# Kernel tuning notes

Hardware: AMD Instinct MI355X
Metric: run time of the kernel (lower is better)

## Reference

```python
import jax, jax.numpy as jnp
import numpy as np

SIREN_OMEGA_0 = 30.0
EPS = 1e-4


def setup_inputs() -> dict:
    key = jax.random.key(0)
    ks = jax.random.split(key, 10)
    B, N, M, IN, OUT = 2, 16384, 1024, 256, 256
    x = jax.random.normal(ks[0], (B, N, IN), dtype=jnp.float32)
    query_coords = jax.random.normal(ks[1], (B, N, 3), dtype=jnp.float32)
    atomic_coords = jax.random.normal(ks[2], (B, M, 3), dtype=jnp.float32)
    # SIREN init (not is_first): bound = sqrt(6/in)/omega_0
    bound = (6.0 / IN) ** 0.5 / SIREN_OMEGA_0
    W = jax.random.uniform(ks[3], (OUT, IN), jnp.float32, -bound, bound)
    b = jax.random.uniform(ks[4], (OUT,), jnp.float32, -bound, bound)
    # freq_net: Linear(3,16) -> Softplus -> Linear(16,1), default torch init
    b1l = 1.0 / np.sqrt(3.0)
    fw1 = jax.random.uniform(ks[5], (16, 3), jnp.float32, -b1l, b1l)
    fb1 = jax.random.uniform(ks[6], (16,), jnp.float32, -b1l, b1l)
    b2l = 1.0 / np.sqrt(16.0)
    fw2 = jax.random.uniform(ks[7], (1, 16), jnp.float32, -b2l, b2l)
    fb2 = jax.random.uniform(ks[8], (1,), jnp.float32, -b2l, b2l)
    return {"x": x, "query_coords": query_coords, "atomic_coords": atomic_coords,
            "W": W, "b": b, "fw1": fw1, "fb1": fb1, "fw2": fw2, "fb2": fb2}


def reference(x, query_coords, atomic_coords, W, b, fw1, fb1, fw2, fb2):
    omega_base = SIREN_OMEGA_0
    # pre_activation = x @ W^T + b : [B, N, OUT]
    pre = jnp.einsum('bni,oi->bno', x, W) + b
    # freq_net(query_coords): Linear -> softplus -> Linear, clamp [0,5], nan->0
    h = jax.nn.softplus(jnp.einsum('bnd,hd->bnh', query_coords, fw1) + fb1)
    local_scale = jnp.einsum('bnh,oh->bno', h, fw2) + fb2  # [B, N, 1]
    local_scale = jnp.nan_to_num(jnp.clip(local_scale, 0.0, 5.0), nan=0.0)
    # pairwise distance [B, N, M] via broadcasted diff, then min over atoms
    diff = query_coords[:, :, None, :] - atomic_coords[:, None, :, :]  # [B,N,M,3]
    dist = jnp.sqrt(jnp.maximum(jnp.sum(diff * diff, axis=-1), EPS))
    min_dist = jnp.min(dist, axis=-1, keepdims=True)  # [B, N, 1]
    omega = omega_base * (1.0 + local_scale * jnp.exp(-min_dist))
    return jnp.sin(omega * pre)
```

## Files before the change

### kernel.cpp

```cpp
#include <hip/hip_runtime.h>
#include <hip/hip_bf16.h>

#define NPTS    32768
#define K_DIM   256
#define O_DIM   256
#define M_ATOMS 1024

typedef __attribute__((ext_vector_type(8))) short short8;
typedef __attribute__((ext_vector_type(4))) float f32x4;

__device__ __forceinline__ void split1(float v, short* h, short* l) {
  unsigned short hu = __bfloat16_as_ushort(__float2bfloat16(v));
  *h = (short)hu;
  float r = v - __uint_as_float((unsigned)hu << 16);
  *l = (short)__bfloat16_as_ushort(__float2bfloat16(r));
}

__device__ __forceinline__ void cvt8(const f32x4 f0, const f32x4 f1,
                                     short8* h, short8* l) {
#pragma unroll
  for (int j = 0; j < 4; ++j) {
    short hh, ll;
    split1(f0[j], &hh, &ll);
    (*h)[j] = hh; (*l)[j] = ll;
    split1(f1[j], &hh, &ll);
    (*h)[j + 4] = hh; (*l)[j + 4] = ll;
  }
}

__global__ __launch_bounds__(256) void wprep_kernel(const float* __restrict__ W,
                                                    unsigned short* __restrict__ whF,
                                                    unsigned short* __restrict__ wlF) {
  int t = blockIdx.x * 256 + threadIdx.x;
  int lane = t & 63;
  int ct = (t >> 6) & 15;
  int kc = t >> 10;
  int col = ct * 16 + (lane & 15);
  int k0 = kc * 32 + (lane >> 4) * 8;
  const float* src = W + (size_t)col * K_DIM + k0;
  f32x4 f0 = *(const f32x4*)(src);
  f32x4 f1 = *(const f32x4*)(src + 4);
  short8 h, l;
  cvt8(f0, f1, &h, &l);
  *(short8*)(whF + (size_t)t * 8) = h;
  *(short8*)(wlF + (size_t)t * 8) = l;
}

__global__ __launch_bounds__(256, 2) void fused_kernel(
    const float* __restrict__ x, const float* __restrict__ qc,
    const float* __restrict__ atoms,
    const unsigned short* __restrict__ whF, const unsigned short* __restrict__ wlF,
    const float* __restrict__ bias,
    const float* __restrict__ fw1, const float* __restrict__ fb1,
    const float* __restrict__ fw2, const float* __restrict__ fb2,
    float* __restrict__ out) {
  __shared__ f32x4 at4[M_ATOMS];
  __shared__ float red[4][64];
  __shared__ float omg[64];

  const int tid = threadIdx.x;
  const int lane = tid & 63;
  const int w = tid >> 6;
  const int lrow = lane & 15;
  const int lk = lane >> 4;
  const int pbase = blockIdx.x * 64;

  const short8* BH = (const short8*)whF + (size_t)(w * 4) * 64 + lane;
  const short8* BL = (const short8*)wlF + (size_t)(w * 4) * 64 + lane;
  short8 bh[4], bl[4], nh[4], nl[4];
#pragma unroll
  for (int ct = 0; ct < 4; ++ct) {
    bh[ct] = BH[ct * 64];
    bl[ct] = BL[ct * 64];
  }
  const float* xr = x + (size_t)(pbase + lrow) * K_DIM + lk * 8;
  f32x4 r0[4], r1[4];
#pragma unroll
  for (int t = 0; t < 4; ++t) {
    r0[t] = *(const f32x4*)(xr + t * 16 * K_DIM);
    r1[t] = *(const f32x4*)(xr + t * 16 * K_DIM + 4);
  }

  const int batch = pbase >> 14;
  const float* A = atoms + (size_t)batch * M_ATOMS * 3;
#pragma unroll
  for (int j = 0; j < 4; ++j) {
    int i = tid + j * 256;
    const float* ap = A + (size_t)i * 3;
    float ax = ap[0], ay = ap[1], az = ap[2];
    at4[i] = (f32x4){ax, ay, az, ax * ax + ay * ay + az * az};
  }
  __syncthreads();

  const int pt = pbase + lane;
  const float qx = qc[(size_t)pt * 3 + 0];
  const float qy = qc[(size_t)pt * 3 + 1];
  const float qz = qc[(size_t)pt * 3 + 2];
  {
    float m0 = 3.0e38f, m1 = 3.0e38f, m2 = 3.0e38f, m3 = 3.0e38f;
    const int i0 = w * 256;
    for (int i = i0; i < i0 + 256; i += 4) {
      f32x4 v0 = at4[i + 0], v1 = at4[i + 1], v2 = at4[i + 2], v3 = at4[i + 3];
      float d;
      d = v0[0] * qx; d = __fmaf_rn(v0[1], qy, d); d = __fmaf_rn(v0[2], qz, d);
      m0 = fminf(m0, __fmaf_rn(d, -2.0f, v0[3]));
      d = v1[0] * qx; d = __fmaf_rn(v1[1], qy, d); d = __fmaf_rn(v1[2], qz, d);
      m1 = fminf(m1, __fmaf_rn(d, -2.0f, v1[3]));
      d = v2[0] * qx; d = __fmaf_rn(v2[1], qy, d); d = __fmaf_rn(v2[2], qz, d);
      m2 = fminf(m2, __fmaf_rn(d, -2.0f, v2[3]));
      d = v3[0] * qx; d = __fmaf_rn(v3[1], qy, d); d = __fmaf_rn(v3[2], qz, d);
      m3 = fminf(m3, __fmaf_rn(d, -2.0f, v3[3]));
    }
    red[w][lane] = fminf(fminf(m0, m1), fminf(m2, m3));
  }
  __syncthreads();
  if (w == 0) {
    float md = fminf(fminf(red[0][lane], red[1][lane]),
                     fminf(red[2][lane], red[3][lane]));
    md += qx * qx + qy * qy + qz * qz;
    float mind = sqrtf(fmaxf(md, 1.0e-4f));
    float facc = fb2[0];
#pragma unroll
    for (int j = 0; j < 16; ++j) {
      float z = fw1[j * 3 + 0] * qx + fw1[j * 3 + 1] * qy + fw1[j * 3 + 2] * qz + fb1[j];
      facc += fw2[j] * (fmaxf(z, 0.0f) + __logf(1.0f + __expf(-fabsf(z))));
    }
    float ls = fminf(fmaxf(facc, 0.0f), 5.0f);
    omg[lane] = 30.0f * (1.0f + ls * __expf(-mind));
  }
  __syncthreads();

  short8 ahi[4], alo[4];
#pragma unroll
  for (int t = 0; t < 4; ++t) cvt8(r0[t], r1[t], &ahi[t], &alo[t]);

  f32x4 acc[4][4];
#pragma unroll
  for (int t = 0; t < 4; ++t)
#pragma unroll
    for (int ct = 0; ct < 4; ++ct) acc[t][ct] = (f32x4){0.f, 0.f, 0.f, 0.f};

#pragma unroll 2
  for (int kc = 0; kc < 8; ++kc) {
    if (kc < 7) {
#pragma unroll
      for (int ct = 0; ct < 4; ++ct) {
        nh[ct] = BH[(kc + 1) * 1024 + ct * 64];
        nl[ct] = BL[(kc + 1) * 1024 + ct * 64];
      }
#pragma unroll
      for (int t = 0; t < 4; ++t) {
        r0[t] = *(const f32x4*)(xr + t * 16 * K_DIM + (kc + 1) * 32);
        r1[t] = *(const f32x4*)(xr + t * 16 * K_DIM + (kc + 1) * 32 + 4);
      }
    }
#pragma unroll
    for (int ct = 0; ct < 4; ++ct)
#pragma unroll
      for (int t = 0; t < 4; ++t)
        acc[t][ct] = __builtin_amdgcn_mfma_f32_16x16x32_bf16(ahi[t], bh[ct], acc[t][ct], 0, 0, 0);
#pragma unroll
    for (int ct = 0; ct < 4; ++ct)
#pragma unroll
      for (int t = 0; t < 4; ++t)
        acc[t][ct] = __builtin_amdgcn_mfma_f32_16x16x32_bf16(alo[t], bh[ct], acc[t][ct], 0, 0, 0);
#pragma unroll
    for (int ct = 0; ct < 4; ++ct)
#pragma unroll
      for (int t = 0; t < 4; ++t)
        acc[t][ct] = __builtin_amdgcn_mfma_f32_16x16x32_bf16(ahi[t], bl[ct], acc[t][ct], 0, 0, 0);
    if (kc < 7) {
#pragma unroll
      for (int t = 0; t < 4; ++t) cvt8(r0[t], r1[t], &ahi[t], &alo[t]);
#pragma unroll
      for (int ct = 0; ct < 4; ++ct) { bh[ct] = nh[ct]; bl[ct] = nl[ct]; }
    }
  }

#pragma unroll
  for (int ct = 0; ct < 4; ++ct) {
    float bv = bias[w * 64 + ct * 16 + lrow];
#pragma unroll
    for (int t = 0; t < 4; ++t) {
#pragma unroll
      for (int j = 0; j < 4; ++j) {
        float om = omg[t * 16 + lk * 4 + j];
        float pre = acc[t][ct][j] + bv;
        out[(size_t)(pbase + t * 16 + lk * 4 + j) * O_DIM + w * 64 + ct * 16 + lrow] =
            __sinf(om * pre);
      }
    }
  }
}

extern "C" void kernel_launch(void* const* d_in, const int* in_sizes, int n_in,
                              void* d_out, int out_size, void* d_ws, size_t ws_size,
                              hipStream_t stream) {
  (void)in_sizes; (void)n_in; (void)out_size; (void)ws_size;
  const float* x     = (const float*)d_in[0];
  const float* qc    = (const float*)d_in[1];
  const float* atoms = (const float*)d_in[2];
  const float* W     = (const float*)d_in[3];
  const float* b     = (const float*)d_in[4];
  const float* fw1   = (const float*)d_in[5];
  const float* fb1   = (const float*)d_in[6];
  const float* fw2   = (const float*)d_in[7];
  const float* fb2   = (const float*)d_in[8];
  float* out = (float*)d_out;

  unsigned short* whF = (unsigned short*)d_ws;
  unsigned short* wlF = whF + 65536;

  wprep_kernel<<<32, 256, 0, stream>>>(W, whF, wlF);
  fused_kernel<<<512, 256, 0, stream>>>(x, qc, atoms, whF, wlF, b,
                                        fw1, fb1, fw2, fb2, out);
}
```

Measured before the change: 121.3 us.

## Split fused kernel into omega, x-prep and LDS-staged split-bf16 GEMM kernels

Breaks the monolithic kernel into three stages. The first computes omega per point, the second pre-converts x into hi/lo bf16 fragment layout in a workspace, and the third is a GEMM+sin kernel. That GEMM stages W tiles into double-buffered LDS via global_load_lds and uses 128x128 tiles per block, with higher occupancy. The aim is to keep the serial min-distance prologue off the GEMM path and to raise occupancy and W reuse. The cost is an extra round trip of x through memory as bf16 hi/lo (same bytes as fp32) plus extra launches.

```diff
diff --git a/kernel.cpp b/kernel.cpp
--- a/kernel.cpp
+++ b/kernel.cpp
@@ -26,6 +26,12 @@
     split1(f1[j], &hh, &ll);
     (*h)[j + 4] = hh; (*l)[j + 4] = ll;
   }
+}
+
+__device__ __forceinline__ void async16(void* l, const void* g) {
+  __builtin_amdgcn_global_load_lds(
+      (const __attribute__((address_space(1))) void*)g,
+      (__attribute__((address_space(3))) void*)l, 16, 0, 0);
 }
 
 __global__ __launch_bounds__(256) void wprep_kernel(const float* __restrict__ W,
@@ -46,73 +52,43 @@
   *(short8*)(wlF + (size_t)t * 8) = l;
 }
 
-__global__ __launch_bounds__(256, 2) void fused_kernel(
-    const float* __restrict__ x, const float* __restrict__ qc,
-    const float* __restrict__ atoms,
-    const unsigned short* __restrict__ whF, const unsigned short* __restrict__ wlF,
-    const float* __restrict__ bias,
+__global__ __launch_bounds__(256) void omega_kernel(
+    const float* __restrict__ qc, const float* __restrict__ atoms,
     const float* __restrict__ fw1, const float* __restrict__ fb1,
     const float* __restrict__ fw2, const float* __restrict__ fb2,
-    float* __restrict__ out) {
+    float* __restrict__ omg) {
   __shared__ f32x4 at4[M_ATOMS];
   __shared__ float red[4][64];
-  __shared__ float omg[64];
-
-  const int tid = threadIdx.x;
-  const int lane = tid & 63;
-  const int w = tid >> 6;
-  const int lrow = lane & 15;
-  const int lk = lane >> 4;
-  const int pbase = blockIdx.x * 64;
-
-  const short8* BH = (const short8*)whF + (size_t)(w * 4) * 64 + lane;
-  const short8* BL = (const short8*)wlF + (size_t)(w * 4) * 64 + lane;
-  short8 bh[4], bl[4], nh[4], nl[4];
-#pragma unroll
-  for (int ct = 0; ct < 4; ++ct) {
-    bh[ct] = BH[ct * 64];
-    bl[ct] = BL[ct * 64];
-  }
-  const float* xr = x + (size_t)(pbase + lrow) * K_DIM + lk * 8;
-  f32x4 r0[4], r1[4];
-#pragma unroll
-  for (int t = 0; t < 4; ++t) {
-    r0[t] = *(const f32x4*)(xr + t * 16 * K_DIM);
-    r1[t] = *(const f32x4*)(xr + t * 16 * K_DIM + 4);
-  }
-
-  const int batch = pbase >> 14;
+  const int base = blockIdx.x * 64;
+  const int batch = base >> 14;
   const float* A = atoms + (size_t)batch * M_ATOMS * 3;
-#pragma unroll
-  for (int j = 0; j < 4; ++j) {
-    int i = tid + j * 256;
-    const float* ap = A + (size_t)i * 3;
+  for (int i = threadIdx.x; i < M_ATOMS; i += 256) {
+    const float* ap = A + i * 3;
     float ax = ap[0], ay = ap[1], az = ap[2];
     at4[i] = (f32x4){ax, ay, az, ax * ax + ay * ay + az * az};
   }
   __syncthreads();
-
-  const int pt = pbase + lane;
+  const int lane = threadIdx.x & 63;
+  const int w = threadIdx.x >> 6;
+  const int pt = base + lane;
   const float qx = qc[(size_t)pt * 3 + 0];
   const float qy = qc[(size_t)pt * 3 + 1];
   const float qz = qc[(size_t)pt * 3 + 2];
-  {
-    float m0 = 3.0e38f, m1 = 3.0e38f, m2 = 3.0e38f, m3 = 3.0e38f;
-    const int i0 = w * 256;
-    for (int i = i0; i < i0 + 256; i += 4) {
-      f32x4 v0 = at4[i + 0], v1 = at4[i + 1], v2 = at4[i + 2], v3 = at4[i + 3];
-      float d;
-      d = v0[0] * qx; d = __fmaf_rn(v0[1], qy, d); d = __fmaf_rn(v0[2], qz, d);
-      m0 = fminf(m0, __fmaf_rn(d, -2.0f, v0[3]));
-      d = v1[0] * qx; d = __fmaf_rn(v1[1], qy, d); d = __fmaf_rn(v1[2], qz, d);
-      m1 = fminf(m1, __fmaf_rn(d, -2.0f, v1[3]));
-      d = v2[0] * qx; d = __fmaf_rn(v2[1], qy, d); d = __fmaf_rn(v2[2], qz, d);
-      m2 = fminf(m2, __fmaf_rn(d, -2.0f, v2[3]));
-      d = v3[0] * qx; d = __fmaf_rn(v3[1], qy, d); d = __fmaf_rn(v3[2], qz, d);
-      m3 = fminf(m3, __fmaf_rn(d, -2.0f, v3[3]));
-    }
-    red[w][lane] = fminf(fminf(m0, m1), fminf(m2, m3));
-  }
+  float m0 = 3.0e38f, m1 = 3.0e38f, m2 = 3.0e38f, m3 = 3.0e38f;
+  const int i0 = w * 256;
+  for (int i = i0; i < i0 + 256; i += 4) {
+    f32x4 v0 = at4[i + 0], v1 = at4[i + 1], v2 = at4[i + 2], v3 = at4[i + 3];
+    float d;
+    d = v0[0] * qx; d = __fmaf_rn(v0[1], qy, d); d = __fmaf_rn(v0[2], qz, d);
+    m0 = fminf(m0, __fmaf_rn(d, -2.0f, v0[3]));
+    d = v1[0] * qx; d = __fmaf_rn(v1[1], qy, d); d = __fmaf_rn(v1[2], qz, d);
+    m1 = fminf(m1, __fmaf_rn(d, -2.0f, v1[3]));
+    d = v2[0] * qx; d = __fmaf_rn(v2[1], qy, d); d = __fmaf_rn(v2[2], qz, d);
+    m2 = fminf(m2, __fmaf_rn(d, -2.0f, v2[3]));
+    d = v3[0] * qx; d = __fmaf_rn(v3[1], qy, d); d = __fmaf_rn(v3[2], qz, d);
+    m3 = fminf(m3, __fmaf_rn(d, -2.0f, v3[3]));
+  }
+  red[w][lane] = fminf(fminf(m0, m1), fminf(m2, m3));
   __syncthreads();
   if (w == 0) {
     float md = fminf(fminf(red[0][lane], red[1][lane]),
@@ -126,68 +102,120 @@
       facc += fw2[j] * (fmaxf(z, 0.0f) + __logf(1.0f + __expf(-fabsf(z))));
     }
     float ls = fminf(fmaxf(facc, 0.0f), 5.0f);
-    omg[lane] = 30.0f * (1.0f + ls * __expf(-mind));
-  }
+    omg[pt] = 30.0f * (1.0f + ls * __expf(-mind));
+  }
+}
+
+__global__ __launch_bounds__(256) void xprep_kernel(const float* __restrict__ x,
+                                                    unsigned short* __restrict__ xh,
+                                                    unsigned short* __restrict__ xl) {
+  int u = blockIdx.x * 256 + threadIdx.x;
+  int lane = u & 63;
+  int kc = (u >> 6) & 7;
+  int rt = u >> 9;
+  int row = rt * 16 + (lane & 15);
+  int k0 = kc * 32 + (lane >> 4) * 8;
+  const float* src = x + (size_t)row * K_DIM + k0;
+  f32x4 f0 = *(const f32x4*)(src);
+  f32x4 f1 = *(const f32x4*)(src + 4);
+  short8 h, l;
+  cvt8(f0, f1, &h, &l);
+  *(short8*)(xh + (size_t)u * 8) = h;
+  *(short8*)(xl + (size_t)u * 8) = l;
+}
+
+__global__ __launch_bounds__(256, 4) void gemm_sin_kernel(
+    const unsigned short* __restrict__ xh, const unsigned short* __restrict__ xl,
+    const unsigned short* __restrict__ whF, const unsigned short* __restrict__ wlF,
+    const float* __restrict__ omg, const float* __restrict__ bias,
+    float* __restrict__ out) {
+  __shared__ short8 bsh[2][2][8][64];
+  const int lane = threadIdx.x & 63;
+  const int w = threadIdx.x >> 6;
+  const int lrow = lane & 15;
+  const int lk = lane >> 4;
+  const int rb = blockIdx.x >> 1;
+  const int ch = blockIdx.x & 1;
+
+  const char* whB = (const char*)whF + ch * 8192;
+  const char* wlB = (const char*)wlF + ch * 8192;
+  {
+    char* dh = (char*)&bsh[0][0][0][0] + w * 2048;
+    char* dl = (char*)&bsh[0][1][0][0] + w * 2048;
+    const int so = w * 2048 + lane * 16;
+    async16(dh, whB + so);
+    async16(dh + 1024, whB + so + 1024);
+    async16(dl, wlB + so);
+    async16(dl + 1024, wlB + so + 1024);
+  }
+
+  const int rt0 = rb * 8 + w * 2;
+  const short8* AH = (const short8*)xh + (size_t)rt0 * 512 + lane;
+  const short8* AL = (const short8*)xl + (size_t)rt0 * 512 + lane;
+  short8 ah0 = AH[0], ah1 = AH[512];
+  short8 al0 = AL[0], al1 = AL[512];
+
+  f32x4 acc[2][8];
+#pragma unroll
+  for (int t = 0; t < 2; ++t)
+#pragma unroll
+    for (int ct = 0; ct < 8; ++ct) acc[t][ct] = (f32x4){0.f, 0.f, 0.f, 0.f};
+
   __syncthreads();
 
-  short8 ahi[4], alo[4];
-#pragma unroll
-  for (int t = 0; t < 4; ++t) cvt8(r0[t], r1[t], &ahi[t], &alo[t]);
-
-  f32x4 acc[4][4];
-#pragma unroll
-  for (int t = 0; t < 4; ++t)
-#pragma unroll
-    for (int ct = 0; ct < 4; ++ct) acc[t][ct] = (f32x4){0.f, 0.f, 0.f, 0.f};
-
-#pragma unroll 2
+#pragma unroll 1
   for (int kc = 0; kc < 8; ++kc) {
+    const int cur = kc & 1;
+    short8 nh0, nh1, nl0, nl1;
     if (kc < 7) {
-#pragma unroll
-      for (int ct = 0; ct < 4; ++ct) {
-        nh[ct] = BH[(kc + 1) * 1024 + ct * 64];
-        nl[ct] = BL[(kc + 1) * 1024 + ct * 64];
-      }
-#pragma unroll
-      for (int t = 0; t < 4; ++t) {
-        r0[t] = *(const f32x4*)(xr + t * 16 * K_DIM + (kc + 1) * 32);
-        r1[t] = *(const f32x4*)(xr + t * 16 * K_DIM + (kc + 1) * 32 + 4);
-      }
-    }
-#pragma unroll
-    for (int ct = 0; ct < 4; ++ct)
-#pragma unroll
-      for (int t = 0; t < 4; ++t)
-        acc[t][ct] = __builtin_amdgcn_mfma_f32_16x16x32_bf16(ahi[t], bh[ct], acc[t][ct], 0, 0, 0);
-#pragma unroll
-    for (int ct = 0; ct < 4; ++ct)
-#pragma unroll
-      for (int t = 0; t < 4; ++t)
-        acc[t][ct] = __builtin_amdgcn_mfma_f32_16x16x32_bf16(alo[t], bh[ct], acc[t][ct], 0, 0, 0);
-#pragma unroll
-    for (int ct = 0; ct < 4; ++ct)
-#pragma unroll
-      for (int t = 0; t < 4; ++t)
-        acc[t][ct] = __builtin_amdgcn_mfma_f32_16x16x32_bf16(ahi[t], bl[ct], acc[t][ct], 0, 0, 0);
+      char* dh = (char*)&bsh[cur ^ 1][0][0][0] + w * 2048;
+      char* dl = (char*)&bsh[cur ^ 1][1][0][0] + w * 2048;
+      const char* sh = whB + (kc + 1) * 16384 + w * 2048 + lane * 16;
+      const char* sl = wlB + (kc + 1) * 16384 + w * 2048 + lane * 16;
+      async16(dh, sh);
+      async16(dh + 1024, sh + 1024);
+      async16(dl, sl);
+      async16(dl + 1024, sl + 1024);
+      nh0 = AH[(kc + 1) * 64];
+      nh1 = AH[512 + (kc + 1) * 64];
+      nl0 = AL[(kc + 1) * 64];
+      nl1 = AL[512 + (kc + 1) * 64];
+    }
+#pragma unroll
+    for (int ct = 0; ct < 8; ++ct) {
+      short8 bh = bsh[cur][0][ct][lane];
+      short8 bl = bsh[cur][1][ct][lane];
+      acc[0][ct] = __builtin_amdgcn_mfma_f32_16x16x32_bf16(ah0, bh, acc[0][ct], 0, 0, 0);
+      acc[1][ct] = __builtin_amdgcn_mfma_f32_16x16x32_bf16(ah1, bh, acc[1][ct], 0, 0, 0);
+      acc[0][ct] = __builtin_amdgcn_mfma_f32_16x16x32_bf16(al0, bh, acc[0][ct], 0, 0, 0);
+      acc[1][ct] = __builtin_amdgcn_mfma_f32_16x16x32_bf16(al1, bh, acc[1][ct], 0, 0, 0);
+      acc[0][ct] = __builtin_amdgcn_mfma_f32_16x16x32_bf16(ah0, bl, acc[0][ct], 0, 0, 0);
+      acc[1][ct] = __builtin_amdgcn_mfma_f32_16x16x32_bf16(ah1, bl, acc[1][ct], 0, 0, 0);
+    }
     if (kc < 7) {
-#pragma unroll
-      for (int t = 0; t < 4; ++t) cvt8(r0[t], r1[t], &ahi[t], &alo[t]);
-#pragma unroll
-      for (int ct = 0; ct < 4; ++ct) { bh[ct] = nh[ct]; bl[ct] = nl[ct]; }
-    }
-  }
-
-#pragma unroll
-  for (int ct = 0; ct < 4; ++ct) {
-    float bv = bias[w * 64 + ct * 16 + lrow];
-#pragma unroll
-    for (int t = 0; t < 4; ++t) {
+      ah0 = nh0; ah1 = nh1; al0 = nl0; al1 = nl1;
+    }
+    __syncthreads();
+  }
+
+  const int rowbase = rb * 128 + w * 32;
+  float om[2][4];
+#pragma unroll
+  for (int t = 0; t < 2; ++t)
+#pragma unroll
+    for (int j = 0; j < 4; ++j)
+      om[t][j] = omg[rowbase + t * 16 + lk * 4 + j];
+
+#pragma unroll
+  for (int ct = 0; ct < 8; ++ct) {
+    float bv = bias[ch * 128 + ct * 16 + lrow];
+#pragma unroll
+    for (int t = 0; t < 2; ++t) {
 #pragma unroll
       for (int j = 0; j < 4; ++j) {
-        float om = omg[t * 16 + lk * 4 + j];
         float pre = acc[t][ct][j] + bv;
-        out[(size_t)(pbase + t * 16 + lk * 4 + j) * O_DIM + w * 64 + ct * 16 + lrow] =
-            __sinf(om * pre);
+        out[(size_t)(rowbase + t * 16 + lk * 4 + j) * O_DIM + ch * 128 + ct * 16 + lrow] =
+            __sinf(om[t][j] * pre);
       }
     }
   }
@@ -208,10 +236,15 @@
   const float* fb2   = (const float*)d_in[8];
   float* out = (float*)d_out;
 
-  unsigned short* whF = (unsigned short*)d_ws;
-  unsigned short* wlF = whF + 65536;
+  char* p = (char*)d_ws;
+  unsigned short* whF = (unsigned short*)p;          p += 131072;
+  unsigned short* wlF = (unsigned short*)p;          p += 131072;
+  float* omg          = (float*)p;                   p += 131072;
+  unsigned short* xh  = (unsigned short*)p;          p += (size_t)NPTS * K_DIM * 2;
+  unsigned short* xl  = (unsigned short*)p;
 
   wprep_kernel<<<32, 256, 0, stream>>>(W, whF, wlF);
-  fused_kernel<<<512, 256, 0, stream>>>(x, qc, atoms, whF, wlF, b,
-                                        fw1, fb1, fw2, fb2, out);
-}
+  omega_kernel<<<512, 256, 0, stream>>>(qc, atoms, fw1, fb1, fw2, fb2, omg);
+  xprep_kernel<<<4096, 256, 0, stream>>>(x, xh, xl);
+  gemm_sin_kernel<<<512, 256, 0, stream>>>(xh, xl, whF, wlF, omg, b, out);
+}
```

Result: slower. 125.5 us (+3.5%).
